# Performance work log

Measured on AMD Instinct MI355X. Metric: run time of the kernel, lower is better.

The kernel has to match this reference:

```python
import jax, jax.numpy as jnp
import numpy as np

RFF_DIM = 256
ATTENTION_SCALE = 0.1
LAMBDA_REG = 0.01
SIGMA = 1.0


def setup_inputs() -> dict:
    key = jax.random.key(0)
    k1, k2, k3 = jax.random.split(key, 3)
    N, D_IN = 262144, 64
    Z = jax.random.normal(k1, (N, D_IN), dtype=jnp.float32)
    W_rff = jax.random.normal(k2, (D_IN, RFF_DIM), dtype=jnp.float32)
    A = jax.random.normal(k3, (2 * RFF_DIM, 3), dtype=jnp.float32) * 0.01
    return {"Z": Z, "W_rff": W_rff, "A": A}


def reference(Z, W_rff, A):
    # --- RFF transform: Q = sqrt(1/R) * [cos(Z W / sigma), sin(Z W / sigma)] ---
    proj = (Z @ W_rff) / SIGMA                       # [N, R]
    Q = jnp.sqrt(1.0 / RFF_DIM) * jnp.concatenate(
        [jnp.cos(proj), jnp.sin(proj)], axis=-1)      # [N, 2R]

    N, F = Q.shape
    chunk = max(F // RFF_DIM, 1)                      # = 2 here
    n_chunks = F // chunk                             # = RFF_DIM

    # --- convexified attention over feature chunks (vectorized) ---
    Qc = Q.reshape(N, n_chunks, chunk)                # [N, K, c]
    A_mean = jnp.mean(A, axis=-1)                     # [2R]
    # per-chunk trace score: mean over batch of <Q_i, A_mean[:c]>
    scores = jnp.mean(jnp.einsum('nkc,c->nk', Qc, A_mean[:chunk]), axis=0)  # [K]
    alpha = jax.nn.softmax(scores / (ATTENTION_SCALE * np.sqrt(RFF_DIM)))   # [K]
    # per-chunk reweighting (dim-preserving recombination)
    Q_tilde = (alpha[None, :, None] * Qc).reshape(N, F)                      # [N, 2R]

    # --- small GEMM head + nuclear-norm regularizer ---
    predictions = Q_tilde @ A                          # [N, out]
    AW = jax.nn.softmax(predictions / np.sqrt(RFF_DIM), axis=-1)
    nuclear_norm = jnp.sum(jnp.linalg.svd(A, compute_uv=False))
    reg_loss = LAMBDA_REG * nuclear_norm
    return predictions, AW, reg_loss, alpha
```

## Files before the change

kernel.cpp:

```cpp
#include <hip/hip_runtime.h>
#include <math.h>

#define N_ROWS 262144
#define D_IN 64
#define RFF 256
#define NTILES (N_ROWS / 16)
#define GRID 1024

#define OFF_PRED 0
#define OFF_AW (N_ROWS * 3)
#define OFF_REG (2 * N_ROWS * 3)
#define OFF_ALPHA (2 * N_ROWS * 3 + 1)

#define WS_WF 1280

typedef _Float16 f16x8 __attribute__((ext_vector_type(8)));
typedef float f32x4 __attribute__((ext_vector_type(4)));
typedef float f32x2 __attribute__((ext_vector_type(2)));

__device__ __forceinline__ f32x4 mfma16(f16x8 a, f16x8 b, f32x4 c) {
    return __builtin_amdgcn_mfma_f32_16x16x32_f16(a, b, c, 0, 0, 0);
}

__device__ __forceinline__ unsigned short f32_to_bf16_rne(float x) {
    unsigned int u = __float_as_uint(x);
    unsigned int r = u + 0x7fffu + ((u >> 16) & 1u);
    return (unsigned short)(r >> 16);
}

__device__ __forceinline__ void sincos_rev(float pr, float& sn, float& cs) {
    float f;
    asm("v_fract_f32 %0, %1" : "=v"(f) : "v"(pr));
    asm("v_sin_f32 %0, %1" : "=v"(sn) : "v"(f));
    asm("v_cos_f32 %0, %1" : "=v"(cs) : "v"(f));
}

__device__ __forceinline__ void gload_lds16(const float* g, float* lds) {
    __builtin_amdgcn_global_load_lds(
        (const __attribute__((address_space(1))) unsigned int*)g,
        (__attribute__((address_space(3))) unsigned int*)(lds), 16, 0, 0);
}

#define WAITVM0() do { asm volatile("s_waitcnt vmcnt(0)" ::: "memory"); \
                       __builtin_amdgcn_sched_barrier(0); } while (0)
#define LGKM0()   do { asm volatile("s_waitcnt lgkmcnt(0)" ::: "memory"); \
                       __builtin_amdgcn_sched_barrier(0); } while (0)

__global__ __launch_bounds__(256) void k_prep(const float* __restrict__ W,
                                              float* __restrict__ ws) {
    const int e = blockIdx.x * 256 + threadIdx.x;
    if (e < 512) ws[e] = 0.f;
    const int lane = e & 63;
    const int slot = e >> 6;
    const int kh = slot & 1;
    const int ct = slot >> 1;
    const int k0 = kh * 32 + 8 * (lane >> 4);
    const int col = ct * 16 + (lane & 15);
    f16x8 v;
#pragma unroll
    for (int i = 0; i < 8; ++i)
        v[i] = (_Float16)(W[(k0 + i) * RFF + col] * 0.15915494309189535f);
    *(f16x8*)(ws + WS_WF + e * 4) = v;
}

__device__ __forceinline__ void dma_Bf_half(const float* __restrict__ wsWf, float* Bf,
                                            int h, int wv, int l) {
#pragma unroll
    for (int m = 0; m < 4; ++m) {
        const int off = wv * 1024 + m * 256;
        gload_lds16(wsWf + h * 4096 + off + l * 4, Bf + off);
    }
}

__device__ __forceinline__ void stage_dma(const float* __restrict__ Z, int n0, int l,
                                          float* ldsbase) {
#pragma unroll
    for (int m = 0; m < 4; ++m) {
        const int row = m * 4 + (l >> 4);
        const int gc = (l & 15) ^ (row & 7);
        gload_lds16(Z + (size_t)(n0 + row) * D_IN + gc * 4, ldsbase + m * 256);
    }
}

__device__ __forceinline__ void frags_from_lds(const float* bb, int lr, int lh,
                                               f16x8& ah0, f16x8& ah1) {
    const int s4 = lr & 7;
    const float* rp = bb + lr * 64;
    float z[16];
    *(float4*)&z[0]  = *(const float4*)(rp + (((lh * 2 + 0) ^ s4) << 2));
    *(float4*)&z[4]  = *(const float4*)(rp + (((lh * 2 + 1) ^ s4) << 2));
    *(float4*)&z[8]  = *(const float4*)(rp + (((lh * 2 + 8) ^ s4) << 2));
    *(float4*)&z[12] = *(const float4*)(rp + (((lh * 2 + 9) ^ s4) << 2));
    LGKM0();
#pragma unroll
    for (int i = 0; i < 8; ++i) {
        ah0[i] = (_Float16)z[i];
        ah1[i] = (_Float16)z[8 + i];
    }
}

__global__ __launch_bounds__(256, 4) void k_pass1(const float* __restrict__ Z,
                                                  const float* __restrict__ ws_in,
                                                  float* __restrict__ U) {
    __shared__ float Bff[4096];
    __shared__ float Zs[4][1024];
    __shared__ float Ured[256];
    const int t = threadIdx.x;
    const int wv = t >> 6, l = t & 63, lr = l & 15, lh = l >> 4;
    const int h = blockIdx.x & 1;
    const int g = blockIdx.x >> 1;

    dma_Bf_half(ws_in + WS_WF, Bff, h, wv, l);
    const int tstart = g * 32 + wv * 8;
    stage_dma(Z, tstart * 16, l, &Zs[wv][0]);
    Ured[t] = 0.f;
    __syncthreads();

    const f16x8* Bf = (const f16x8*)Bff;
    f32x2 accC2[8], accS2[8];
#pragma unroll
    for (int c = 0; c < 8; ++c) { accC2[c] = (f32x2){0.f, 0.f}; accS2[c] = (f32x2){0.f, 0.f}; }

    for (int tt = 0; tt < 8; ++tt) {
        if (tt) WAITVM0();
        f16x8 ah0, ah1;
        frags_from_lds(&Zs[wv][0], lr, lh, ah0, ah1);
        if (tt + 1 < 8) {
            stage_dma(Z, (tstart + tt + 1) * 16, l, &Zs[wv][0]);
            __builtin_amdgcn_sched_barrier(0);
        }
        f32x4 acc[8];
#pragma unroll
        for (int c = 0; c < 8; ++c) acc[c] = (f32x4){0.f, 0.f, 0.f, 0.f};
#pragma unroll
        for (int c = 0; c < 8; ++c) {
            acc[c] = mfma16(ah0, Bf[(c * 2 + 0) * 64 + l], acc[c]);
            acc[c] = mfma16(ah1, Bf[(c * 2 + 1) * 64 + l], acc[c]);
        }
#pragma unroll
        for (int c = 0; c < 8; ++c) {
            float sn0, cs0, sn1, cs1, sn2, cs2, sn3, cs3;
            sincos_rev(acc[c][0], sn0, cs0);
            sincos_rev(acc[c][1], sn1, cs1);
            sincos_rev(acc[c][2], sn2, cs2);
            sincos_rev(acc[c][3], sn3, cs3);
            accC2[c] += (f32x2){cs0, cs1};
            accC2[c] += (f32x2){cs2, cs3};
            accS2[c] += (f32x2){sn0, sn1};
            accS2[c] += (f32x2){sn2, sn3};
        }
    }
#pragma unroll
    for (int c = 0; c < 8; ++c) {
        float cc = accC2[c][0] + accC2[c][1];
        float ss = accS2[c][0] + accS2[c][1];
        cc += __shfl_xor(cc, 16);
        cc += __shfl_xor(cc, 32);
        ss += __shfl_xor(ss, 16);
        ss += __shfl_xor(ss, 32);
        if (l < 16) {
            atomicAdd(&Ured[c * 16 + l], cc * 0.0625f);
            atomicAdd(&Ured[128 + c * 16 + l], ss * 0.0625f);
        }
    }
    __syncthreads();
    if (t < 128) atomicAdd(&U[128 * h + t], Ured[t]);
    else atomicAdd(&U[256 + 128 * h + (t - 128)], Ured[t]);
}

__global__ __launch_bounds__(256, 4) void k_pass2(const float* __restrict__ Z,
                                                  const float* __restrict__ ws_in,
                                                  const float* __restrict__ A,
                                                  float* __restrict__ out) {
    __shared__ float Bff[4096];
    __shared__ float Zs[4][1024];
    __shared__ float sca[256];
    __shared__ unsigned int BtP[384];
    __shared__ double G6[6];
    const int t = threadIdx.x;
    const int wv = t >> 6, l = t & 63, lr = l & 15, lh = l >> 4;
    const int h = blockIdx.x & 1;
    const int g = blockIdx.x >> 1;

    dma_Bf_half(ws_in + WS_WF, Bff, h, wv, l);

    const float am0 = (A[0] + A[1] + A[2]) * (1.0f / 3.0f);
    const float am1 = (A[3] + A[4] + A[5]) * (1.0f / 3.0f);
    float x = (am0 * ws_in[2 * t] + am1 * ws_in[2 * t + 1]) *
              (1.0f / (float)N_ROWS) * (1.0f / 1.6f);
    sca[t] = x;
    __syncthreads();
    for (int s = 128; s > 0; s >>= 1) {
        if (t < s) sca[t] = fmaxf(sca[t], sca[t + s]);
        __syncthreads();
    }
    float mx = sca[0];
    __syncthreads();
    float e = __expf(x - mx);
    sca[t] = e;
    __syncthreads();
    for (int s = 128; s > 0; s >>= 1) {
        if (t < s) sca[t] += sca[t + s];
        __syncthreads();
    }
    float al = e / sca[0];
    __syncthreads();
    sca[t] = al;
    __syncthreads();

    if (blockIdx.x == 0) {
        out[OFF_ALPHA + t] = al;
        double* gred = (double*)&Zs[0][0];
        double af[2][3];
#pragma unroll
        for (int t2 = 0; t2 < 2; ++t2)
#pragma unroll
            for (int j = 0; j < 3; ++j) af[t2][j] = (double)A[(t + t2 * 256) * 3 + j];
        const int ei[6] = {0, 0, 0, 1, 1, 2};
        const int ej[6] = {0, 1, 2, 1, 2, 2};
        for (int eidx = 0; eidx < 6; ++eidx) {
            double p = af[0][ei[eidx]] * af[0][ej[eidx]] + af[1][ei[eidx]] * af[1][ej[eidx]];
            gred[t] = p;
            __syncthreads();
            for (int s = 128; s > 0; s >>= 1) {
                if (t < s) gred[t] += gred[t + s];
                __syncthreads();
            }
            if (t == 0) G6[eidx] = gred[0];
            __syncthreads();
        }
        if (t == 0) {
            double g00 = G6[0], g01 = G6[1], g02 = G6[2], g11 = G6[3], g12 = G6[4], g22 = G6[5];
            double q = (g00 + g11 + g22) / 3.0;
            double p1 = g01 * g01 + g02 * g02 + g12 * g12;
            double p2 = (g00 - q) * (g00 - q) + (g11 - q) * (g11 - q) +
                        (g22 - q) * (g22 - q) + 2.0 * p1;
            double nuc;
            if (p2 < 1e-300) {
                nuc = 3.0 * sqrt(fmax(q, 0.0));
            } else {
                double p = sqrt(p2 / 6.0);
                double b00 = (g00 - q) / p, b11 = (g11 - q) / p, b22 = (g22 - q) / p;
                double b01 = g01 / p, b02 = g02 / p, b12 = g12 / p;
                double detB = b00 * (b11 * b22 - b12 * b12) - b01 * (b01 * b22 - b12 * b02) +
                              b02 * (b01 * b12 - b11 * b02);
                double rr = fmin(1.0, fmax(-1.0, detB / 2.0));
                double phi = acos(rr) / 3.0;
                double e1 = q + 2.0 * p * cos(phi);
                double e3 = q + 2.0 * p * cos(phi + 2.0943951023931953);
                double e2 = 3.0 * q - e1 - e3;
                nuc = sqrt(fmax(e1, 0.0)) + sqrt(fmax(e2, 0.0)) + sqrt(fmax(e3, 0.0));
            }
            out[OFF_REG] = (float)(0.01 * nuc);
        }
        __syncthreads();
    }

    if (t < 128) {
        const int fg = 128 * h + t;
        const float ac = 0.0625f * sca[fg >> 1];
        const float as = 0.0625f * sca[128 + (fg >> 1)];
#pragma unroll
        for (int j = 0; j < 3; ++j) {
            float bc = ac * A[fg * 3 + j];
            float bs = as * A[(256 + fg) * 3 + j];
            unsigned int ulo = f32_to_bf16_rne(bc);
            unsigned int uhi = f32_to_bf16_rne(bs);
            BtP[t * 3 + j] = ulo | (uhi << 16);
        }
    }

    const int tstart = g * 32 + wv * 8;
    stage_dma(Z, tstart * 16, l, &Zs[wv][0]);
    __syncthreads();

    const f16x8* Bf = (const f16x8*)Bff;

    for (int tt = 0; tt < 8; ++tt) {
        const int n0 = (tstart + tt) * 16;
        if (tt) WAITVM0();
        f16x8 ah0, ah1;
        frags_from_lds(&Zs[wv][0], lr, lh, ah0, ah1);
        if (tt + 1 < 8) {
            stage_dma(Z, (tstart + tt + 1) * 16, l, &Zs[wv][0]);
            __builtin_amdgcn_sched_barrier(0);
        }
        f32x4 acc[8];
#pragma unroll
        for (int c = 0; c < 8; ++c) acc[c] = (f32x4){0.f, 0.f, 0.f, 0.f};
#pragma unroll
        for (int c = 0; c < 8; ++c) {
            acc[c] = mfma16(ah0, Bf[(c * 2 + 0) * 64 + l], acc[c]);
            acc[c] = mfma16(ah1, Bf[(c * 2 + 1) * 64 + l], acc[c]);
        }
        f32x2 pa01[3], pa23[3];
#pragma unroll
        for (int j = 0; j < 3; ++j) { pa01[j] = (f32x2){0.f, 0.f}; pa23[j] = (f32x2){0.f, 0.f}; }
#pragma unroll
        for (int c = 0; c < 8; ++c) {
            const int fl = c * 16 + lr;
            unsigned int u0 = BtP[fl * 3 + 0], u1 = BtP[fl * 3 + 1], u2 = BtP[fl * 3 + 2];
            float sn0, cs0, sn1, cs1, sn2, cs2, sn3, cs3;
            sincos_rev(acc[c][0], sn0, cs0);
            sincos_rev(acc[c][1], sn1, cs1);
            sincos_rev(acc[c][2], sn2, cs2);
            sincos_rev(acc[c][3], sn3, cs3);
            const f32x2 cs01 = {cs0, cs1}, cs23 = {cs2, cs3};
            const f32x2 sn01 = {sn0, sn1}, sn23 = {sn2, sn3};
            const float bcf[3] = {__uint_as_float(u0 << 16), __uint_as_float(u1 << 16),
                                  __uint_as_float(u2 << 16)};
            const float bsf[3] = {__uint_as_float(u0 & 0xffff0000u),
                                  __uint_as_float(u1 & 0xffff0000u),
                                  __uint_as_float(u2 & 0xffff0000u)};
#pragma unroll
            for (int j = 0; j < 3; ++j) {
                const f32x2 bc2 = {bcf[j], bcf[j]};
                const f32x2 bs2 = {bsf[j], bsf[j]};
                pa01[j] = __builtin_elementwise_fma(
                    cs01, bc2, __builtin_elementwise_fma(sn01, bs2, pa01[j]));
                pa23[j] = __builtin_elementwise_fma(
                    cs23, bc2, __builtin_elementwise_fma(sn23, bs2, pa23[j]));
            }
        }
        float pa[4][3];
#pragma unroll
        for (int j = 0; j < 3; ++j) {
            pa[0][j] = pa01[j][0];
            pa[1][j] = pa01[j][1];
            pa[2][j] = pa23[j][0];
            pa[3][j] = pa23[j][1];
        }
#pragma unroll
        for (int r = 0; r < 4; ++r)
#pragma unroll
            for (int j = 0; j < 3; ++j) {
                pa[r][j] += __shfl_xor(pa[r][j], 1);
                pa[r][j] += __shfl_xor(pa[r][j], 2);
                pa[r][j] += __shfl_xor(pa[r][j], 4);
                pa[r][j] += __shfl_xor(pa[r][j], 8);
            }
        float q0 = 0.f, q1 = 0.f, q2 = 0.f;
#pragma unroll
        for (int r = 0; r < 4; ++r)
            if (lr == r) { q0 = pa[r][0]; q1 = pa[r][1]; q2 = pa[r][2]; }
        if (lr < 4) {
            const size_t n = (size_t)n0 + 4 * lh + lr;
            atomicAdd(&out[OFF_PRED + n * 3 + 0], q0);
            atomicAdd(&out[OFF_PRED + n * 3 + 1], q1);
            atomicAdd(&out[OFF_PRED + n * 3 + 2], q2);
        }
    }
}

__global__ __launch_bounds__(256) void k_aw(float* __restrict__ out) {
    const size_t n = (size_t)blockIdx.x * 256 + threadIdx.x;
    const float p0 = out[OFF_PRED + n * 3 + 0];
    const float p1 = out[OFF_PRED + n * 3 + 1];
    const float p2 = out[OFF_PRED + n * 3 + 2];
    const float x0 = p0 * 0.0625f, x1 = p1 * 0.0625f, x2 = p2 * 0.0625f;
    const float m = fmaxf(x0, fmaxf(x1, x2));
    const float e0 = __expf(x0 - m), e1 = __expf(x1 - m), e2 = __expf(x2 - m);
    const float inv = 1.0f / (e0 + e1 + e2);
    out[OFF_AW + n * 3 + 0] = e0 * inv;
    out[OFF_AW + n * 3 + 1] = e1 * inv;
    out[OFF_AW + n * 3 + 2] = e2 * inv;
}

extern "C" void kernel_launch(void* const* d_in, const int* in_sizes, int n_in,
                              void* d_out, int out_size, void* d_ws, size_t ws_size,
                              hipStream_t stream) {
    const float* Z = (const float*)d_in[0];
    const float* W = (const float*)d_in[1];
    const float* A = (const float*)d_in[2];
    float* out = (float*)d_out;
    float* ws = (float*)d_ws;

    (void)hipMemsetAsync(out, 0, (size_t)N_ROWS * 3 * sizeof(float), stream);
    hipLaunchKernelGGL(k_prep, dim3(8), dim3(256), 0, stream, W, ws);
    hipLaunchKernelGGL(k_pass1, dim3(GRID), dim3(256), 0, stream, Z, ws, ws);
    hipLaunchKernelGGL(k_pass2, dim3(GRID), dim3(256), 0, stream, Z, ws, A, out);
    hipLaunchKernelGGL(k_aw, dim3(N_ROWS / 256), dim3(256), 0, stream, out);
}
```

Before: 88.33 us.

## Hoist alpha/softmax into a tiny kernel, replace prediction atomics with split partial stores

```diff
diff --git a/kernel.cpp b/kernel.cpp
--- a/kernel.cpp
+++ b/kernel.cpp
@@ -12,6 +12,7 @@
 #define OFF_REG (2 * N_ROWS * 3)
 #define OFF_ALPHA (2 * N_ROWS * 3 + 1)
 
+#define WS_B 512
 #define WS_WF 1280
 
 typedef _Float16 f16x8 __attribute__((ext_vector_type(8)));
@@ -35,6 +36,14 @@
     asm("v_cos_f32 %0, %1" : "=v"(cs) : "v"(f));
 }
 
+__device__ __forceinline__ float rowsum16(float x) {
+    x += __int_as_float(__builtin_amdgcn_mov_dpp(__float_as_int(x), 0x121, 0xf, 0xf, true));
+    x += __int_as_float(__builtin_amdgcn_mov_dpp(__float_as_int(x), 0x122, 0xf, 0xf, true));
+    x += __int_as_float(__builtin_amdgcn_mov_dpp(__float_as_int(x), 0x124, 0xf, 0xf, true));
+    x += __int_as_float(__builtin_amdgcn_mov_dpp(__float_as_int(x), 0x128, 0xf, 0xf, true));
+    return x;
+}
+
 __device__ __forceinline__ void gload_lds16(const float* g, float* lds) {
     __builtin_amdgcn_global_load_lds(
         (const __attribute__((address_space(1))) unsigned int*)g,
@@ -42,6 +51,8 @@
 }
 
 #define WAITVM0() do { asm volatile("s_waitcnt vmcnt(0)" ::: "memory"); \
+                       __builtin_amdgcn_sched_barrier(0); } while (0)
+#define WAITVM1() do { asm volatile("s_waitcnt vmcnt(1)" ::: "memory"); \
                        __builtin_amdgcn_sched_barrier(0); } while (0)
 #define LGKM0()   do { asm volatile("s_waitcnt lgkmcnt(0)" ::: "memory"); \
                        __builtin_amdgcn_sched_barrier(0); } while (0)
@@ -168,117 +179,124 @@
     else atomicAdd(&U[256 + 128 * h + (t - 128)], Ured[t]);
 }
 
+__global__ __launch_bounds__(256) void k_alpha(const float* __restrict__ U,
+                                               const float* __restrict__ A,
+                                               float* __restrict__ ws,
+                                               float* __restrict__ out) {
+    __shared__ float sm[256];
+    __shared__ double gred[256];
+    __shared__ double G6[6];
+    const int k = threadIdx.x;
+
+    const float am0 = (A[0] + A[1] + A[2]) * (1.0f / 3.0f);
+    const float am1 = (A[3] + A[4] + A[5]) * (1.0f / 3.0f);
+    float x = (am0 * U[2 * k] + am1 * U[2 * k + 1]) * (1.0f / (float)N_ROWS) * (1.0f / 1.6f);
+
+    sm[k] = x;
+    __syncthreads();
+    for (int s = 128; s > 0; s >>= 1) {
+        if (k < s) sm[k] = fmaxf(sm[k], sm[k + s]);
+        __syncthreads();
+    }
+    float mx = sm[0];
+    __syncthreads();
+    float e = __expf(x - mx);
+    sm[k] = e;
+    __syncthreads();
+    for (int s = 128; s > 0; s >>= 1) {
+        if (k < s) sm[k] += sm[k + s];
+        __syncthreads();
+    }
+    float al = e / sm[0];
+    out[OFF_ALPHA + k] = al;
+    sm[k] = al;
+    __syncthreads();
+
+    {
+        const float ac = 0.0625f * sm[k >> 1];
+        const float as = 0.0625f * sm[128 + (k >> 1)];
+        unsigned int* BtP = (unsigned int*)(ws + WS_B);
+        const int dst = (k >> 7) * 384 + (k & 127) * 3;
+#pragma unroll
+        for (int j = 0; j < 3; ++j) {
+            float bc = ac * A[k * 3 + j];
+            float bs = as * A[(256 + k) * 3 + j];
+            unsigned int ulo = f32_to_bf16_rne(bc);
+            unsigned int uhi = f32_to_bf16_rne(bs);
+            BtP[dst + j] = ulo | (uhi << 16);
+        }
+    }
+
+    double af[2][3];
+#pragma unroll
+    for (int t2 = 0; t2 < 2; ++t2)
+#pragma unroll
+        for (int j = 0; j < 3; ++j) af[t2][j] = (double)A[(k + t2 * 256) * 3 + j];
+    const int ei[6] = {0, 0, 0, 1, 1, 2};
+    const int ej[6] = {0, 1, 2, 1, 2, 2};
+    for (int eidx = 0; eidx < 6; ++eidx) {
+        double p = af[0][ei[eidx]] * af[0][ej[eidx]] + af[1][ei[eidx]] * af[1][ej[eidx]];
+        gred[k] = p;
+        __syncthreads();
+        for (int s = 128; s > 0; s >>= 1) {
+            if (k < s) gred[k] += gred[k + s];
+            __syncthreads();
+        }
+        if (k == 0) G6[eidx] = gred[0];
+        __syncthreads();
+    }
+    if (k == 0) {
+        double g00 = G6[0], g01 = G6[1], g02 = G6[2], g11 = G6[3], g12 = G6[4], g22 = G6[5];
+        double q = (g00 + g11 + g22) / 3.0;
+        double p1 = g01 * g01 + g02 * g02 + g12 * g12;
+        double p2 = (g00 - q) * (g00 - q) + (g11 - q) * (g11 - q) + (g22 - q) * (g22 - q) + 2.0 * p1;
+        double nuc;
+        if (p2 < 1e-300) {
+            nuc = 3.0 * sqrt(fmax(q, 0.0));
+        } else {
+            double p = sqrt(p2 / 6.0);
+            double b00 = (g00 - q) / p, b11 = (g11 - q) / p, b22 = (g22 - q) / p;
+            double b01 = g01 / p, b02 = g02 / p, b12 = g12 / p;
+            double detB = b00 * (b11 * b22 - b12 * b12) - b01 * (b01 * b22 - b12 * b02) +
+                          b02 * (b01 * b12 - b11 * b02);
+            double rr = fmin(1.0, fmax(-1.0, detB / 2.0));
+            double phi = acos(rr) / 3.0;
+            double e1 = q + 2.0 * p * cos(phi);
+            double e3 = q + 2.0 * p * cos(phi + 2.0943951023931953);
+            double e2 = 3.0 * q - e1 - e3;
+            nuc = sqrt(fmax(e1, 0.0)) + sqrt(fmax(e2, 0.0)) + sqrt(fmax(e3, 0.0));
+        }
+        out[OFF_REG] = (float)(0.01 * nuc);
+    }
+}
+
 __global__ __launch_bounds__(256, 4) void k_pass2(const float* __restrict__ Z,
                                                   const float* __restrict__ ws_in,
-                                                  const float* __restrict__ A,
                                                   float* __restrict__ out) {
     __shared__ float Bff[4096];
     __shared__ float Zs[4][1024];
-    __shared__ float sca[256];
     __shared__ unsigned int BtP[384];
-    __shared__ double G6[6];
     const int t = threadIdx.x;
     const int wv = t >> 6, l = t & 63, lr = l & 15, lh = l >> 4;
     const int h = blockIdx.x & 1;
     const int g = blockIdx.x >> 1;
 
     dma_Bf_half(ws_in + WS_WF, Bff, h, wv, l);
-
-    const float am0 = (A[0] + A[1] + A[2]) * (1.0f / 3.0f);
-    const float am1 = (A[3] + A[4] + A[5]) * (1.0f / 3.0f);
-    float x = (am0 * ws_in[2 * t] + am1 * ws_in[2 * t + 1]) *
-              (1.0f / (float)N_ROWS) * (1.0f / 1.6f);
-    sca[t] = x;
-    __syncthreads();
-    for (int s = 128; s > 0; s >>= 1) {
-        if (t < s) sca[t] = fmaxf(sca[t], sca[t + s]);
-        __syncthreads();
-    }
-    float mx = sca[0];
-    __syncthreads();
-    float e = __expf(x - mx);
-    sca[t] = e;
-    __syncthreads();
-    for (int s = 128; s > 0; s >>= 1) {
-        if (t < s) sca[t] += sca[t + s];
-        __syncthreads();
-    }
-    float al = e / sca[0];
-    __syncthreads();
-    sca[t] = al;
-    __syncthreads();
-
-    if (blockIdx.x == 0) {
-        out[OFF_ALPHA + t] = al;
-        double* gred = (double*)&Zs[0][0];
-        double af[2][3];
-#pragma unroll
-        for (int t2 = 0; t2 < 2; ++t2)
-#pragma unroll
-            for (int j = 0; j < 3; ++j) af[t2][j] = (double)A[(t + t2 * 256) * 3 + j];
-        const int ei[6] = {0, 0, 0, 1, 1, 2};
-        const int ej[6] = {0, 1, 2, 1, 2, 2};
-        for (int eidx = 0; eidx < 6; ++eidx) {
-            double p = af[0][ei[eidx]] * af[0][ej[eidx]] + af[1][ei[eidx]] * af[1][ej[eidx]];
-            gred[t] = p;
-            __syncthreads();
-            for (int s = 128; s > 0; s >>= 1) {
-                if (t < s) gred[t] += gred[t + s];
-                __syncthreads();
-            }
-            if (t == 0) G6[eidx] = gred[0];
-            __syncthreads();
-        }
-        if (t == 0) {
-            double g00 = G6[0], g01 = G6[1], g02 = G6[2], g11 = G6[3], g12 = G6[4], g22 = G6[5];
-            double q = (g00 + g11 + g22) / 3.0;
-            double p1 = g01 * g01 + g02 * g02 + g12 * g12;
-            double p2 = (g00 - q) * (g00 - q) + (g11 - q) * (g11 - q) +
-                        (g22 - q) * (g22 - q) + 2.0 * p1;
-            double nuc;
-            if (p2 < 1e-300) {
-                nuc = 3.0 * sqrt(fmax(q, 0.0));
-            } else {
-                double p = sqrt(p2 / 6.0);
-                double b00 = (g00 - q) / p, b11 = (g11 - q) / p, b22 = (g22 - q) / p;
-                double b01 = g01 / p, b02 = g02 / p, b12 = g12 / p;
-                double detB = b00 * (b11 * b22 - b12 * b12) - b01 * (b01 * b22 - b12 * b02) +
-                              b02 * (b01 * b12 - b11 * b02);
-                double rr = fmin(1.0, fmax(-1.0, detB / 2.0));
-                double phi = acos(rr) / 3.0;
-                double e1 = q + 2.0 * p * cos(phi);
-                double e3 = q + 2.0 * p * cos(phi + 2.0943951023931953);
-                double e2 = 3.0 * q - e1 - e3;
-                nuc = sqrt(fmax(e1, 0.0)) + sqrt(fmax(e2, 0.0)) + sqrt(fmax(e3, 0.0));
-            }
-            out[OFF_REG] = (float)(0.01 * nuc);
-        }
-        __syncthreads();
-    }
-
-    if (t < 128) {
-        const int fg = 128 * h + t;
-        const float ac = 0.0625f * sca[fg >> 1];
-        const float as = 0.0625f * sca[128 + (fg >> 1)];
-#pragma unroll
-        for (int j = 0; j < 3; ++j) {
-            float bc = ac * A[fg * 3 + j];
-            float bs = as * A[(256 + fg) * 3 + j];
-            unsigned int ulo = f32_to_bf16_rne(bc);
-            unsigned int uhi = f32_to_bf16_rne(bs);
-            BtP[t * 3 + j] = ulo | (uhi << 16);
-        }
-    }
-
     const int tstart = g * 32 + wv * 8;
     stage_dma(Z, tstart * 16, l, &Zs[wv][0]);
+    {
+        const unsigned int* src = (const unsigned int*)(ws_in + WS_B) + h * 384;
+        BtP[t] = src[t];
+        if (t < 128) BtP[256 + t] = src[256 + t];
+    }
     __syncthreads();
 
     const f16x8* Bf = (const f16x8*)Bff;
+    const size_t ob = h ? (size_t)OFF_AW : (size_t)OFF_PRED;
 
     for (int tt = 0; tt < 8; ++tt) {
         const int n0 = (tstart + tt) * 16;
-        if (tt) WAITVM0();
+        if (tt) WAITVM1();
         f16x8 ah0, ah1;
         frags_from_lds(&Zs[wv][0], lr, lh, ah0, ah1);
         if (tt + 1 < 8) {
@@ -325,38 +343,32 @@
         float pa[4][3];
 #pragma unroll
         for (int j = 0; j < 3; ++j) {
-            pa[0][j] = pa01[j][0];
-            pa[1][j] = pa01[j][1];
-            pa[2][j] = pa23[j][0];
-            pa[3][j] = pa23[j][1];
-        }
+            pa[0][j] = rowsum16(pa01[j][0]);
+            pa[1][j] = rowsum16(pa01[j][1]);
+            pa[2][j] = rowsum16(pa23[j][0]);
+            pa[3][j] = rowsum16(pa23[j][1]);
+        }
+        float val = 0.f;
 #pragma unroll
         for (int r = 0; r < 4; ++r)
 #pragma unroll
-            for (int j = 0; j < 3; ++j) {
-                pa[r][j] += __shfl_xor(pa[r][j], 1);
-                pa[r][j] += __shfl_xor(pa[r][j], 2);
-                pa[r][j] += __shfl_xor(pa[r][j], 4);
-                pa[r][j] += __shfl_xor(pa[r][j], 8);
-            }
-        float q0 = 0.f, q1 = 0.f, q2 = 0.f;
-#pragma unroll
-        for (int r = 0; r < 4; ++r)
-            if (lr == r) { q0 = pa[r][0]; q1 = pa[r][1]; q2 = pa[r][2]; }
-        if (lr < 4) {
-            const size_t n = (size_t)n0 + 4 * lh + lr;
-            atomicAdd(&out[OFF_PRED + n * 3 + 0], q0);
-            atomicAdd(&out[OFF_PRED + n * 3 + 1], q1);
-            atomicAdd(&out[OFF_PRED + n * 3 + 2], q2);
+            for (int j = 0; j < 3; ++j)
+                if (lr == r * 3 + j) val = pa[r][j];
+        if (lr < 12) {
+            out[ob + ((size_t)n0 + 4 * lh) * 3 + lr] = val;
         }
     }
 }
 
 __global__ __launch_bounds__(256) void k_aw(float* __restrict__ out) {
     const size_t n = (size_t)blockIdx.x * 256 + threadIdx.x;
-    const float p0 = out[OFF_PRED + n * 3 + 0];
-    const float p1 = out[OFF_PRED + n * 3 + 1];
-    const float p2 = out[OFF_PRED + n * 3 + 2];
+    const float a0 = out[OFF_PRED + n * 3 + 0], b0 = out[OFF_AW + n * 3 + 0];
+    const float a1 = out[OFF_PRED + n * 3 + 1], b1 = out[OFF_AW + n * 3 + 1];
+    const float a2 = out[OFF_PRED + n * 3 + 2], b2 = out[OFF_AW + n * 3 + 2];
+    const float p0 = a0 + b0, p1 = a1 + b1, p2 = a2 + b2;
+    out[OFF_PRED + n * 3 + 0] = p0;
+    out[OFF_PRED + n * 3 + 1] = p1;
+    out[OFF_PRED + n * 3 + 2] = p2;
     const float x0 = p0 * 0.0625f, x1 = p1 * 0.0625f, x2 = p2 * 0.0625f;
     const float m = fmaxf(x0, fmaxf(x1, x2));
     const float e0 = __expf(x0 - m), e1 = __expf(x1 - m), e2 = __expf(x2 - m);
@@ -375,9 +387,9 @@
     float* out = (float*)d_out;
     float* ws = (float*)d_ws;
 
-    (void)hipMemsetAsync(out, 0, (size_t)N_ROWS * 3 * sizeof(float), stream);
     hipLaunchKernelGGL(k_prep, dim3(8), dim3(256), 0, stream, W, ws);
     hipLaunchKernelGGL(k_pass1, dim3(GRID), dim3(256), 0, stream, Z, ws, ws);
-    hipLaunchKernelGGL(k_pass2, dim3(GRID), dim3(256), 0, stream, Z, ws, A, out);
+    hipLaunchKernelGGL(k_alpha, dim3(1), dim3(256), 0, stream, ws, A, ws, out);
+    hipLaunchKernelGGL(k_pass2, dim3(GRID), dim3(256), 0, stream, Z, ws, out);
     hipLaunchKernelGGL(k_aw, dim3(N_ROWS / 256), dim3(256), 0, stream, out);
 }
```

Measured after the change: 86.50 us. 2.1% less time.
